# Performance work log

Hardware: AMD Instinct MI355X
Metric: run time of the kernel (lower is better)

Reference implementation:

```python
import jax, jax.numpy as jnp
import numpy as np

N_NODES = 100000
N_EDGES = 1600000
NODE_FEATURES = 6
H_EMBED = 64
D = 32
OUT_DIM = 1


def _mlp(x, W1, b1, W2, b2):
    h = jnp.tanh(x @ W1 + b1)
    return jnp.tanh(h @ W2 + b2)


def _gcn_conv(h, W, b, src, dst, n_nodes):
    # PyG GCNConv: linear (no bias) -> add self-loops -> sym-normalized scatter-add -> +bias
    hw = h @ W  # [N, D]
    loop = jnp.arange(n_nodes, dtype=src.dtype)
    row = jnp.concatenate([src, loop])  # sources
    col = jnp.concatenate([dst, loop])  # targets
    ones = jnp.ones(row.shape[0], dtype=hw.dtype)
    deg = jax.ops.segment_sum(ones, col, num_segments=n_nodes)
    dinv = jnp.where(deg > 0, jax.lax.rsqrt(deg), 0.0)
    norm = dinv[row] * dinv[col]  # [E+N]
    msg = hw[row] * norm[:, None]  # gather + scale
    out = jax.ops.segment_sum(msg, col, num_segments=n_nodes)
    return out + b


def setup_inputs() -> dict:
    key = jax.random.key(0)
    ks = jax.random.split(key, 16)
    x = jax.random.normal(ks[0], (N_NODES, NODE_FEATURES), dtype=jnp.float32)
    edge_index = jax.random.randint(ks[1], (2, N_EDGES), 0, N_NODES, dtype=jnp.int64)

    def lin(k, din, dout):
        bound = 1.0 / np.sqrt(din)
        kw, kb = jax.random.split(k)
        W = jax.random.uniform(kw, (din, dout), minval=-bound, maxval=bound, dtype=jnp.float32)
        b = jax.random.uniform(kb, (dout,), minval=-bound, maxval=bound, dtype=jnp.float32)
        return W, b

    We1, be1 = lin(ks[2], NODE_FEATURES, H_EMBED)
    We2, be2 = lin(ks[3], H_EMBED, D)
    Wg1, bg1 = lin(ks[4], D, D)
    Wg2, bg2 = lin(ks[5], D, D)
    Wp1, bp1 = lin(ks[6], D, D)
    Wp2, bp2 = lin(ks[7], D, OUT_DIM)
    return {
        "x": x, "edge_index": edge_index,
        "We1": We1, "be1": be1, "We2": We2, "be2": be2,
        "Wg1": Wg1, "bg1": bg1, "Wg2": Wg2, "bg2": bg2,
        "Wp1": Wp1, "bp1": bp1, "Wp2": Wp2, "bp2": bp2,
    }


def reference(x, edge_index, We1, be1, We2, be2, Wg1, bg1, Wg2, bg2, Wp1, bp1, Wp2, bp2):
    n = x.shape[0]
    src, dst = edge_index[0], edge_index[1]
    h = _mlp(x, We1, be1, We2, be2)            # [N, 32]
    h = jax.nn.relu(_gcn_conv(h, Wg1, bg1, src, dst, n))  # dropout = identity (eval)
    h = jax.nn.relu(_gcn_conv(h, Wg2, bg2, src, dst, n))
    return _mlp(h, Wp1, bp1, Wp2, bp2)         # [N, 1]
```

## Files before the change

### kernel.cpp

```cpp
#include <hip/hip_runtime.h>
#include <hip/hip_fp16.h>

#define NN 100000
#define NE 1600000
#define NPB 128
#define NBUCK ((NN + NPB - 1) / NPB)
#define CAP 4096
#define PBLOCKS 128
#define PTPB 1024
#define EPB (NE / PBLOCKS)
#define DUMMY 100000u
#define SENT 0xFFFFFFFFu

__global__ __launch_bounds__(PTPB) void part_kernel(const int* __restrict__ src,
                                                    const int* __restrict__ dst,
                                                    unsigned int* __restrict__ bcount,
                                                    unsigned int* __restrict__ packed) {
    __shared__ unsigned int lcnt[NBUCK];
    __shared__ unsigned int lcur[NBUCK];
    __shared__ unsigned int lend[NBUCK];
    for (int i = threadIdx.x; i < NBUCK; i += PTPB) lcnt[i] = 0u;
    __syncthreads();
    int e0 = blockIdx.x * EPB;
    for (int e = e0 + threadIdx.x; e < e0 + EPB; e += PTPB)
        atomicAdd(&lcnt[((unsigned)dst[e]) >> 7], 1u);
    __syncthreads();
    for (int i = threadIdx.x; i < NBUCK; i += PTPB) {
        unsigned int c = lcnt[i];
        unsigned int rc = (c + 15u) & ~15u;
        unsigned int base = rc ? atomicAdd(&bcount[i], rc) : 0u;
        lcur[i] = base;
        lend[i] = base + rc;
    }
    __syncthreads();
    for (int e = e0 + threadIdx.x; e < e0 + EPB; e += PTPB) {
        unsigned int d = (unsigned)dst[e];
        unsigned int b = d >> 7;
        unsigned int pos = atomicAdd(&lcur[b], 1u);
        packed[(size_t)b * CAP + pos] = ((d & 127u) << 17) | (unsigned)src[e];
    }
    __syncthreads();
    for (int i = threadIdx.x; i < NBUCK; i += PTPB)
        for (unsigned int j = lcur[i]; j < lend[i]; j++)
            packed[(size_t)i * CAP + j] = SENT;
}

__global__ __launch_bounds__(256) void sort_kernel(const unsigned int* __restrict__ bcount,
                                                   unsigned int* __restrict__ packed,
                                                   unsigned int* __restrict__ row_start,
                                                   unsigned int* __restrict__ degz,
                                                   float* __restrict__ dinv) {
    __shared__ unsigned int lraw[CAP];
    __shared__ unsigned int lsort[CAP];
    __shared__ unsigned int cnt[NPB];
    __shared__ unsigned int ps[NPB];
    __shared__ unsigned int cur[NPB];
    __shared__ unsigned int ntot;
    int b = blockIdx.x;
    int tid = threadIdx.x;
    if (tid < NPB) cnt[tid] = 0u;
    __syncthreads();
    unsigned int n = bcount[b];
    unsigned int* pk = packed + (size_t)b * CAP;
    for (unsigned int i = tid; i < n; i += 256) {
        unsigned int p = pk[i];
        lraw[i] = p;
        if (p != SENT) atomicAdd(&cnt[p >> 17], 1u);
    }
    __syncthreads();
    if (tid < NPB) ps[tid] = (cnt[tid] + 15u) & ~15u;
    __syncthreads();
    for (int off = 1; off < NPB; off <<= 1) {
        unsigned int t = (tid < NPB && tid >= off) ? ps[tid - off] : 0u;
        __syncthreads();
        if (tid < NPB) ps[tid] += t;
        __syncthreads();
    }
    if (tid == NPB - 1) ntot = ps[NPB - 1];
    __syncthreads();
    unsigned int np = ntot;
    for (unsigned int i = tid; i < np; i += 256) lsort[i] = DUMMY;
    if (tid < NPB) cur[tid] = ps[tid] - ((cnt[tid] + 15u) & ~15u);
    __syncthreads();
    for (unsigned int i = tid; i < n; i += 256) {
        unsigned int p = lraw[i];
        if (p != SENT) {
            unsigned int pos = atomicAdd(&cur[p >> 17], 1u);
            lsort[pos] = p & 0x1FFFFu;
        }
    }
    __syncthreads();
    for (unsigned int i = tid; i < np; i += 256) pk[i] = lsort[i];
    if (tid < NPB) {
        int node = b * NPB + tid;
        if (node < NN) {
            unsigned int c = cnt[tid];
            unsigned int pc = (c + 15u) & ~15u;
            row_start[node] = (unsigned int)(b * CAP) + ps[tid] - pc;
            degz[node] = pc;
            dinv[node] = rsqrtf((float)c + 1.0f);
        }
    }
}

__global__ __launch_bounds__(256) void embed_kernel(
    const float* __restrict__ x, const float* __restrict__ We1, const float* __restrict__ be1,
    const float* __restrict__ We2, const float* __restrict__ be2, const float* __restrict__ Wg1,
    const float* __restrict__ dinv, __half* __restrict__ hws1, __half* __restrict__ hws2) {
    __shared__ float sWe1[6 * 64];
    __shared__ float sbe1[64];
    __shared__ float sWe2[64 * 32];
    __shared__ float sbe2[32];
    __shared__ float sWg1[32 * 32];
    for (int i = threadIdx.x; i < 6 * 64; i += 256) sWe1[i] = We1[i];
    for (int i = threadIdx.x; i < 64; i += 256) sbe1[i] = be1[i];
    for (int i = threadIdx.x; i < 64 * 32; i += 256) sWe2[i] = We2[i];
    for (int i = threadIdx.x; i < 32; i += 256) sbe2[i] = be2[i];
    for (int i = threadIdx.x; i < 32 * 32; i += 256) sWg1[i] = Wg1[i];
    __syncthreads();

    int node = blockIdx.x * 256 + threadIdx.x;
    if (node > NN) return;
    if (node == NN) {
        for (int j = 0; j < 32; j++) {
            hws1[(size_t)NN * 32 + j] = __float2half(0.f);
            hws2[(size_t)NN * 32 + j] = __float2half(0.f);
        }
        return;
    }

    float xv[6];
#pragma unroll
    for (int k = 0; k < 6; k++) xv[k] = x[node * 6 + k];

    float h1[64];
#pragma unroll
    for (int j = 0; j < 64; j++) {
        float a = sbe1[j];
#pragma unroll
        for (int k = 0; k < 6; k++) a += xv[k] * sWe1[k * 64 + j];
        h1[j] = tanhf(a);
    }

    float h[32];
#pragma unroll 4
    for (int j = 0; j < 32; j++) {
        float a = sbe2[j];
#pragma unroll
        for (int k = 0; k < 64; k++) a += h1[k] * sWe2[k * 32 + j];
        h[j] = tanhf(a);
    }

    float di = dinv[node];
    __half* o = hws1 + (size_t)node * 32;
#pragma unroll 4
    for (int j = 0; j < 32; j++) {
        float a = 0.f;
#pragma unroll
        for (int k = 0; k < 32; k++) a += h[k] * sWg1[k * 32 + j];
        o[j] = __float2half(a * di);
    }
}

__global__ __launch_bounds__(256) void gather1_kernel(
    const unsigned int* __restrict__ sorted, const unsigned int* __restrict__ row_start,
    const unsigned int* __restrict__ degz, const float* __restrict__ dinv,
    const __half* __restrict__ hws1, const float* __restrict__ bg1,
    const float* __restrict__ Wg2, __half* __restrict__ hws2) {
    __shared__ float sW[32 * 32];
    __shared__ float sb[32];
    for (int i = threadIdx.x; i < 32 * 32; i += 256) sW[i] = Wg2[i];
    if (threadIdx.x < 32) sb[threadIdx.x] = bg1[threadIdx.x];
    __syncthreads();

    int wid = (blockIdx.x * 256 + threadIdx.x) >> 6;
    if (wid >= NN) return;
    int lane = threadIdx.x & 63;
    int g = lane >> 4;
    int p = lane & 15;
    unsigned int base = row_start[wid];
    unsigned int d = degz[wid];
    const __half2* H = (const __half2*)hws1;
    float ax = 0.f, ay = 0.f;
    for (unsigned int k = g; k < d; k += 16) {
        unsigned int s0 = sorted[base + k];
        unsigned int s1 = sorted[base + k + 4];
        unsigned int s2 = sorted[base + k + 8];
        unsigned int s3 = sorted[base + k + 12];
        float2 v0 = __half22float2(H[(size_t)s0 * 16 + p]);
        float2 v1 = __half22float2(H[(size_t)s1 * 16 + p]);
        float2 v2 = __half22float2(H[(size_t)s2 * 16 + p]);
        float2 v3 = __half22float2(H[(size_t)s3 * 16 + p]);
        ax += (v0.x + v1.x) + (v2.x + v3.x);
        ay += (v0.y + v1.y) + (v2.y + v3.y);
    }
    ax += __shfl_xor(ax, 16); ay += __shfl_xor(ay, 16);
    ax += __shfl_xor(ax, 32); ay += __shfl_xor(ay, 32);
    float2 sv = __half22float2(H[(size_t)wid * 16 + p]);
    ax += sv.x; ay += sv.y;
    float di = dinv[wid];
    float hx = di * ax + sb[2 * p];     hx = hx > 0.f ? hx : 0.f;
    float hy = di * ay + sb[2 * p + 1]; hy = hy > 0.f ? hy : 0.f;
    int f = lane & 31;
    float hxe = __shfl(hx, f >> 1);
    float hye = __shfl(hy, f >> 1);
    float h = (f & 1) ? hye : hxe;
    float o = 0.f;
#pragma unroll 8
    for (int k = 0; k < 32; k++) {
        float hk = __shfl(h, k);
        o += hk * sW[k * 32 + f];
    }
    if (lane < 32) hws2[(size_t)wid * 32 + f] = __float2half(o * di);
}

__global__ __launch_bounds__(256) void gather2_kernel(
    const unsigned int* __restrict__ sorted, const unsigned int* __restrict__ row_start,
    const unsigned int* __restrict__ degz, const float* __restrict__ dinv,
    const __half* __restrict__ hws2, const float* __restrict__ bg2,
    const float* __restrict__ Wp1, const float* __restrict__ bp1,
    const float* __restrict__ Wp2, const float* __restrict__ bp2,
    float* __restrict__ out) {
    __shared__ float sW1[32 * 32];
    __shared__ float sbg2[32];
    __shared__ float sb1[32];
    __shared__ float sW2[32];
    __shared__ float sb2;
    for (int i = threadIdx.x; i < 32 * 32; i += 256) sW1[i] = Wp1[i];
    if (threadIdx.x < 32) {
        sbg2[threadIdx.x] = bg2[threadIdx.x];
        sb1[threadIdx.x] = bp1[threadIdx.x];
        sW2[threadIdx.x] = Wp2[threadIdx.x];
    }
    if (threadIdx.x == 0) sb2 = bp2[0];
    __syncthreads();

    int wid = (blockIdx.x * 256 + threadIdx.x) >> 6;
    if (wid >= NN) return;
    int lane = threadIdx.x & 63;
    int g = lane >> 4;
    int p = lane & 15;
    unsigned int base = row_start[wid];
    unsigned int d = degz[wid];
    const __half2* H = (const __half2*)hws2;
    float ax = 0.f, ay = 0.f;
    for (unsigned int k = g; k < d; k += 16) {
        unsigned int s0 = sorted[base + k];
        unsigned int s1 = sorted[base + k + 4];
        unsigned int s2 = sorted[base + k + 8];
        unsigned int s3 = sorted[base + k + 12];
        float2 v0 = __half22float2(H[(size_t)s0 * 16 + p]);
        float2 v1 = __half22float2(H[(size_t)s1 * 16 + p]);
        float2 v2 = __half22float2(H[(size_t)s2 * 16 + p]);
        float2 v3 = __half22float2(H[(size_t)s3 * 16 + p]);
        ax += (v0.x + v1.x) + (v2.x + v3.x);
        ay += (v0.y + v1.y) + (v2.y + v3.y);
    }
    ax += __shfl_xor(ax, 16); ay += __shfl_xor(ay, 16);
    ax += __shfl_xor(ax, 32); ay += __shfl_xor(ay, 32);
    float2 sv = __half22float2(H[(size_t)wid * 16 + p]);
    ax += sv.x; ay += sv.y;
    float di = dinv[wid];
    float hx = di * ax + sbg2[2 * p];     hx = hx > 0.f ? hx : 0.f;
    float hy = di * ay + sbg2[2 * p + 1]; hy = hy > 0.f ? hy : 0.f;
    int f = lane & 31;
    float hxe = __shfl(hx, f >> 1);
    float hye = __shfl(hy, f >> 1);
    float h = (f & 1) ? hye : hxe;
    float pre = sb1[f];
#pragma unroll 8
    for (int k = 0; k < 32; k++) {
        float hk = __shfl(h, k);
        pre += hk * sW1[k * 32 + f];
    }
    float t = tanhf(pre) * sW2[f];
#pragma unroll
    for (int off = 1; off < 32; off <<= 1) t += __shfl_xor(t, off);
    if (lane == 0) out[wid] = tanhf(t + sb2);
}

extern "C" void kernel_launch(void* const* d_in, const int* in_sizes, int n_in,
                              void* d_out, int out_size, void* d_ws, size_t ws_size,
                              hipStream_t stream) {
    const float* x = (const float*)d_in[0];
    const int* edge = (const int*)d_in[1];
    const int* src = edge;
    const int* dst = edge + NE;
    const float* We1 = (const float*)d_in[2];
    const float* be1 = (const float*)d_in[3];
    const float* We2 = (const float*)d_in[4];
    const float* be2 = (const float*)d_in[5];
    const float* Wg1 = (const float*)d_in[6];
    const float* bg1 = (const float*)d_in[7];
    const float* Wg2 = (const float*)d_in[8];
    const float* bg2 = (const float*)d_in[9];
    const float* Wp1 = (const float*)d_in[10];
    const float* bp1 = (const float*)d_in[11];
    const float* Wp2 = (const float*)d_in[12];
    const float* bp2 = (const float*)d_in[13];
    float* out = (float*)d_out;

    unsigned int* bcount = (unsigned int*)d_ws;
    float* dinv = (float*)d_ws + 1024;
    unsigned int* row_start = (unsigned int*)d_ws + 1024 + NN;
    unsigned int* degz = (unsigned int*)d_ws + 1024 + 2 * NN;
    unsigned int* packed = (unsigned int*)d_ws + 1024 + 3 * NN;
    __half* hws1 = (__half*)((unsigned int*)d_ws + 1024 + 3 * NN + NBUCK * CAP);
    __half* hws2 = hws1 + (size_t)(NN + 1) * 32;

    hipMemsetAsync(bcount, 0, 1024 * sizeof(unsigned int), stream);

    int gridN = (NN + 256) / 256;
    int gridG = (NN * 64 + 255) / 256;

    part_kernel<<<PBLOCKS, PTPB, 0, stream>>>(src, dst, bcount, packed);
    sort_kernel<<<NBUCK, 256, 0, stream>>>(bcount, packed, row_start, degz, dinv);
    embed_kernel<<<gridN, 256, 0, stream>>>(x, We1, be1, We2, be2, Wg1, dinv, hws1, hws2);
    gather1_kernel<<<gridG, 256, 0, stream>>>(packed, row_start, degz, dinv, hws1, bg1, Wg2, hws2);
    gather2_kernel<<<gridG, 256, 0, stream>>>(packed, row_start, degz, dinv, hws2, bg2, Wp1, bp1, Wp2, bp2, out);
}
```

Baseline: 307.2 us.

## Use persistent grid-stride gather kernels with register weights and packed row metadata

The two gather kernels become persistent: a fixed grid of 2048 blocks loops over nodes with a grid stride, instead of launching one wave per node. Each lane now holds its weight column in 32 registers loaded once, replacing shared-memory weights and the block barrier. Row start and padded degree are packed into one 32-bit word, so each node needs one metadata load instead of two. This cuts per-block setup and launch overhead, at the cost of higher register pressure and possibly less latency hiding if occupancy falls.

```diff
diff --git a/kernel.cpp b/kernel.cpp
--- a/kernel.cpp
+++ b/kernel.cpp
@@ -11,6 +11,8 @@
 #define EPB (NE / PBLOCKS)
 #define DUMMY 100000u
 #define SENT 0xFFFFFFFFu
+#define GBLK 2048
+#define GWAVES (GBLK * 4)
 
 __global__ __launch_bounds__(PTPB) void part_kernel(const int* __restrict__ src,
                                                     const int* __restrict__ dst,
@@ -47,8 +49,7 @@
 
 __global__ __launch_bounds__(256) void sort_kernel(const unsigned int* __restrict__ bcount,
                                                    unsigned int* __restrict__ packed,
-                                                   unsigned int* __restrict__ row_start,
-                                                   unsigned int* __restrict__ degz,
+                                                   unsigned int* __restrict__ rsd,
                                                    float* __restrict__ dinv) {
     __shared__ unsigned int lraw[CAP];
     __shared__ unsigned int lsort[CAP];
@@ -96,8 +97,8 @@
         if (node < NN) {
             unsigned int c = cnt[tid];
             unsigned int pc = (c + 15u) & ~15u;
-            row_start[node] = (unsigned int)(b * CAP) + ps[tid] - pc;
-            degz[node] = pc;
+            unsigned int rs = (unsigned int)(b * CAP) + ps[tid] - pc;
+            rsd[node] = rs | ((pc >> 4) << 22);
             dinv[node] = rsqrtf((float)c + 1.0f);
         }
     }
@@ -163,120 +164,108 @@
 }
 
 __global__ __launch_bounds__(256) void gather1_kernel(
-    const unsigned int* __restrict__ sorted, const unsigned int* __restrict__ row_start,
-    const unsigned int* __restrict__ degz, const float* __restrict__ dinv,
-    const __half* __restrict__ hws1, const float* __restrict__ bg1,
-    const float* __restrict__ Wg2, __half* __restrict__ hws2) {
-    __shared__ float sW[32 * 32];
-    __shared__ float sb[32];
-    for (int i = threadIdx.x; i < 32 * 32; i += 256) sW[i] = Wg2[i];
-    if (threadIdx.x < 32) sb[threadIdx.x] = bg1[threadIdx.x];
-    __syncthreads();
-
-    int wid = (blockIdx.x * 256 + threadIdx.x) >> 6;
-    if (wid >= NN) return;
+    const unsigned int* __restrict__ sorted, const unsigned int* __restrict__ rsd,
+    const float* __restrict__ dinv, const __half* __restrict__ hws1,
+    const float* __restrict__ bg1, const float* __restrict__ Wg2,
+    __half* __restrict__ hws2) {
     int lane = threadIdx.x & 63;
     int g = lane >> 4;
     int p = lane & 15;
-    unsigned int base = row_start[wid];
-    unsigned int d = degz[wid];
+    int f = lane & 31;
+    float wreg[32];
+#pragma unroll
+    for (int k = 0; k < 32; k++) wreg[k] = Wg2[k * 32 + f];
+    float bf = bg1[f];
+    int wave = (blockIdx.x * 256 + threadIdx.x) >> 6;
     const __half2* H = (const __half2*)hws1;
-    float ax = 0.f, ay = 0.f;
-    for (unsigned int k = g; k < d; k += 16) {
-        unsigned int s0 = sorted[base + k];
-        unsigned int s1 = sorted[base + k + 4];
-        unsigned int s2 = sorted[base + k + 8];
-        unsigned int s3 = sorted[base + k + 12];
-        float2 v0 = __half22float2(H[(size_t)s0 * 16 + p]);
-        float2 v1 = __half22float2(H[(size_t)s1 * 16 + p]);
-        float2 v2 = __half22float2(H[(size_t)s2 * 16 + p]);
-        float2 v3 = __half22float2(H[(size_t)s3 * 16 + p]);
-        ax += (v0.x + v1.x) + (v2.x + v3.x);
-        ay += (v0.y + v1.y) + (v2.y + v3.y);
-    }
-    ax += __shfl_xor(ax, 16); ay += __shfl_xor(ay, 16);
-    ax += __shfl_xor(ax, 32); ay += __shfl_xor(ay, 32);
-    float2 sv = __half22float2(H[(size_t)wid * 16 + p]);
-    ax += sv.x; ay += sv.y;
-    float di = dinv[wid];
-    float hx = di * ax + sb[2 * p];     hx = hx > 0.f ? hx : 0.f;
-    float hy = di * ay + sb[2 * p + 1]; hy = hy > 0.f ? hy : 0.f;
-    int f = lane & 31;
-    float hxe = __shfl(hx, f >> 1);
-    float hye = __shfl(hy, f >> 1);
-    float h = (f & 1) ? hye : hxe;
-    float o = 0.f;
-#pragma unroll 8
-    for (int k = 0; k < 32; k++) {
-        float hk = __shfl(h, k);
-        o += hk * sW[k * 32 + f];
-    }
-    if (lane < 32) hws2[(size_t)wid * 32 + f] = __float2half(o * di);
+    for (int node = wave; node < NN; node += GWAVES) {
+        unsigned int r = rsd[node];
+        unsigned int base = r & 0x3FFFFFu;
+        unsigned int d = (r >> 22) << 4;
+        float ax = 0.f, ay = 0.f;
+        for (unsigned int k = g; k < d; k += 16) {
+            unsigned int s0 = sorted[base + k];
+            unsigned int s1 = sorted[base + k + 4];
+            unsigned int s2 = sorted[base + k + 8];
+            unsigned int s3 = sorted[base + k + 12];
+            float2 v0 = __half22float2(H[(size_t)s0 * 16 + p]);
+            float2 v1 = __half22float2(H[(size_t)s1 * 16 + p]);
+            float2 v2 = __half22float2(H[(size_t)s2 * 16 + p]);
+            float2 v3 = __half22float2(H[(size_t)s3 * 16 + p]);
+            ax += (v0.x + v1.x) + (v2.x + v3.x);
+            ay += (v0.y + v1.y) + (v2.y + v3.y);
+        }
+        ax += __shfl_xor(ax, 16); ay += __shfl_xor(ay, 16);
+        ax += __shfl_xor(ax, 32); ay += __shfl_xor(ay, 32);
+        float2 sv = __half22float2(H[(size_t)node * 16 + p]);
+        ax += sv.x; ay += sv.y;
+        float ae = __shfl(ax, f >> 1);
+        float ao = __shfl(ay, f >> 1);
+        float av = (f & 1) ? ao : ae;
+        float di = dinv[node];
+        float h = di * av + bf;
+        h = h > 0.f ? h : 0.f;
+        float o = 0.f;
+#pragma unroll
+        for (int k = 0; k < 32; k++) o += __shfl(h, k) * wreg[k];
+        if (lane < 32) hws2[(size_t)node * 32 + f] = __float2half(o * di);
+    }
 }
 
 __global__ __launch_bounds__(256) void gather2_kernel(
-    const unsigned int* __restrict__ sorted, const unsigned int* __restrict__ row_start,
-    const unsigned int* __restrict__ degz, const float* __restrict__ dinv,
-    const __half* __restrict__ hws2, const float* __restrict__ bg2,
-    const float* __restrict__ Wp1, const float* __restrict__ bp1,
-    const float* __restrict__ Wp2, const float* __restrict__ bp2,
-    float* __restrict__ out) {
-    __shared__ float sW1[32 * 32];
-    __shared__ float sbg2[32];
-    __shared__ float sb1[32];
-    __shared__ float sW2[32];
-    __shared__ float sb2;
-    for (int i = threadIdx.x; i < 32 * 32; i += 256) sW1[i] = Wp1[i];
-    if (threadIdx.x < 32) {
-        sbg2[threadIdx.x] = bg2[threadIdx.x];
-        sb1[threadIdx.x] = bp1[threadIdx.x];
-        sW2[threadIdx.x] = Wp2[threadIdx.x];
-    }
-    if (threadIdx.x == 0) sb2 = bp2[0];
-    __syncthreads();
-
-    int wid = (blockIdx.x * 256 + threadIdx.x) >> 6;
-    if (wid >= NN) return;
+    const unsigned int* __restrict__ sorted, const unsigned int* __restrict__ rsd,
+    const float* __restrict__ dinv, const __half* __restrict__ hws2,
+    const float* __restrict__ bg2, const float* __restrict__ Wp1,
+    const float* __restrict__ bp1, const float* __restrict__ Wp2,
+    const float* __restrict__ bp2, float* __restrict__ out) {
     int lane = threadIdx.x & 63;
     int g = lane >> 4;
     int p = lane & 15;
-    unsigned int base = row_start[wid];
-    unsigned int d = degz[wid];
+    int f = lane & 31;
+    float wreg[32];
+#pragma unroll
+    for (int k = 0; k < 32; k++) wreg[k] = Wp1[k * 32 + f];
+    float bgf = bg2[f];
+    float b1f = bp1[f];
+    float w2f = Wp2[f];
+    float b2 = bp2[0];
+    int wave = (blockIdx.x * 256 + threadIdx.x) >> 6;
     const __half2* H = (const __half2*)hws2;
-    float ax = 0.f, ay = 0.f;
-    for (unsigned int k = g; k < d; k += 16) {
-        unsigned int s0 = sorted[base + k];
-        unsigned int s1 = sorted[base + k + 4];
-        unsigned int s2 = sorted[base + k + 8];
-        unsigned int s3 = sorted[base + k + 12];
-        float2 v0 = __half22float2(H[(size_t)s0 * 16 + p]);
-        float2 v1 = __half22float2(H[(size_t)s1 * 16 + p]);
-        float2 v2 = __half22float2(H[(size_t)s2 * 16 + p]);
-        float2 v3 = __half22float2(H[(size_t)s3 * 16 + p]);
-        ax += (v0.x + v1.x) + (v2.x + v3.x);
-        ay += (v0.y + v1.y) + (v2.y + v3.y);
-    }
-    ax += __shfl_xor(ax, 16); ay += __shfl_xor(ay, 16);
-    ax += __shfl_xor(ax, 32); ay += __shfl_xor(ay, 32);
-    float2 sv = __half22float2(H[(size_t)wid * 16 + p]);
-    ax += sv.x; ay += sv.y;
-    float di = dinv[wid];
-    float hx = di * ax + sbg2[2 * p];     hx = hx > 0.f ? hx : 0.f;
-    float hy = di * ay + sbg2[2 * p + 1]; hy = hy > 0.f ? hy : 0.f;
-    int f = lane & 31;
-    float hxe = __shfl(hx, f >> 1);
-    float hye = __shfl(hy, f >> 1);
-    float h = (f & 1) ? hye : hxe;
-    float pre = sb1[f];
-#pragma unroll 8
-    for (int k = 0; k < 32; k++) {
-        float hk = __shfl(h, k);
-        pre += hk * sW1[k * 32 + f];
-    }
-    float t = tanhf(pre) * sW2[f];
-#pragma unroll
-    for (int off = 1; off < 32; off <<= 1) t += __shfl_xor(t, off);
-    if (lane == 0) out[wid] = tanhf(t + sb2);
+    for (int node = wave; node < NN; node += GWAVES) {
+        unsigned int r = rsd[node];
+        unsigned int base = r & 0x3FFFFFu;
+        unsigned int d = (r >> 22) << 4;
+        float ax = 0.f, ay = 0.f;
+        for (unsigned int k = g; k < d; k += 16) {
+            unsigned int s0 = sorted[base + k];
+            unsigned int s1 = sorted[base + k + 4];
+            unsigned int s2 = sorted[base + k + 8];
+            unsigned int s3 = sorted[base + k + 12];
+            float2 v0 = __half22float2(H[(size_t)s0 * 16 + p]);
+            float2 v1 = __half22float2(H[(size_t)s1 * 16 + p]);
+            float2 v2 = __half22float2(H[(size_t)s2 * 16 + p]);
+            float2 v3 = __half22float2(H[(size_t)s3 * 16 + p]);
+            ax += (v0.x + v1.x) + (v2.x + v3.x);
+            ay += (v0.y + v1.y) + (v2.y + v3.y);
+        }
+        ax += __shfl_xor(ax, 16); ay += __shfl_xor(ay, 16);
+        ax += __shfl_xor(ax, 32); ay += __shfl_xor(ay, 32);
+        float2 sv = __half22float2(H[(size_t)node * 16 + p]);
+        ax += sv.x; ay += sv.y;
+        float ae = __shfl(ax, f >> 1);
+        float ao = __shfl(ay, f >> 1);
+        float av = (f & 1) ? ao : ae;
+        float di = dinv[node];
+        float h = di * av + bgf;
+        h = h > 0.f ? h : 0.f;
+        float pre = b1f;
+#pragma unroll
+        for (int k = 0; k < 32; k++) pre += __shfl(h, k) * wreg[k];
+        float t = tanhf(pre) * w2f;
+#pragma unroll
+        for (int off = 1; off < 32; off <<= 1) t += __shfl_xor(t, off);
+        if (lane == 0) out[node] = tanhf(t + b2);
+    }
 }
 
 extern "C" void kernel_launch(void* const* d_in, const int* in_sizes, int n_in,
@@ -302,20 +291,18 @@
 
     unsigned int* bcount = (unsigned int*)d_ws;
     float* dinv = (float*)d_ws + 1024;
-    unsigned int* row_start = (unsigned int*)d_ws + 1024 + NN;
-    unsigned int* degz = (unsigned int*)d_ws + 1024 + 2 * NN;
-    unsigned int* packed = (unsigned int*)d_ws + 1024 + 3 * NN;
-    __half* hws1 = (__half*)((unsigned int*)d_ws + 1024 + 3 * NN + NBUCK * CAP);
+    unsigned int* rsd = (unsigned int*)d_ws + 1024 + NN;
+    unsigned int* packed = (unsigned int*)d_ws + 1024 + 2 * NN;
+    __half* hws1 = (__half*)((unsigned int*)d_ws + 1024 + 2 * NN + NBUCK * CAP);
     __half* hws2 = hws1 + (size_t)(NN + 1) * 32;
 
     hipMemsetAsync(bcount, 0, 1024 * sizeof(unsigned int), stream);
 
     int gridN = (NN + 256) / 256;
-    int gridG = (NN * 64 + 255) / 256;
 
     part_kernel<<<PBLOCKS, PTPB, 0, stream>>>(src, dst, bcount, packed);
-    sort_kernel<<<NBUCK, 256, 0, stream>>>(bcount, packed, row_start, degz, dinv);
+    sort_kernel<<<NBUCK, 256, 0, stream>>>(bcount, packed, rsd, dinv);
     embed_kernel<<<gridN, 256, 0, stream>>>(x, We1, be1, We2, be2, Wg1, dinv, hws1, hws2);
-    gather1_kernel<<<gridG, 256, 0, stream>>>(packed, row_start, degz, dinv, hws1, bg1, Wg2, hws2);
-    gather2_kernel<<<gridG, 256, 0, stream>>>(packed, row_start, degz, dinv, hws2, bg2, Wp1, bp1, Wp2, bp2, out);
-}
+    gather1_kernel<<<GBLK, 256, 0, stream>>>(packed, rsd, dinv, hws1, bg1, Wg2, hws2);
+    gather2_kernel<<<GBLK, 256, 0, stream>>>(packed, rsd, dinv, hws2, bg2, Wp1, bp1, Wp2, bp2, out);
+}
```

Measured after the change: 278.9 us. 9.2% less time.
